# Kernel optimization log

Hardware: AMD Instinct MI355X
Metric: run time of the kernel (lower is better)

Reference implementation:

```python
import jax, jax.numpy as jnp
import numpy as np

B, L, E = 4, 2048, 1024
H, D = 16, 64  # heads, head_dim; H*D == E


def setup_inputs() -> dict:
    key = jax.random.key(0)
    ks = jax.random.split(key, 6)
    s = 0.02
    return {
        "x": jax.random.normal(ks[0], (B, L, E), dtype=jnp.float32),
        "Wq": jax.random.normal(ks[1], (E, H * D), dtype=jnp.float32) * s,
        "Wk": jax.random.normal(ks[2], (E, H * D), dtype=jnp.float32) * s,
        "Wv": jax.random.normal(ks[3], (E, H * D), dtype=jnp.float32) * s,
        "Wo": jax.random.normal(ks[4], (H * D, E), dtype=jnp.float32) * s,
        "bo": jax.random.normal(ks[5], (E,), dtype=jnp.float32) * s,
    }


def reference(x, Wq, Wk, Wv, Wo, bo):
    b, l, e = x.shape
    q = (x @ Wq).reshape(b, l, H, D)
    k = (x @ Wk).reshape(b, l, H, D)
    v = (x @ Wv).reshape(b, l, H, D)
    # NOTE: original scales by sqrt(embed_size), not sqrt(head_dim)
    energy = jnp.einsum('nqhd,nkhd->nhqk', q, k)
    attn = jax.nn.softmax(energy / jnp.sqrt(jnp.float32(e)), axis=3)
    out = jnp.einsum('nhql,nlhd->nqhd', attn, v).reshape(b, l, H * D)
    return out @ Wo + bo
```

## Files before the change

kernel.cpp:

```cpp
#include <hip/hip_runtime.h>

#define B_ 4
#define L_ 2048
#define E_ 1024
#define H_ 16
#define D_ 64
#define CSCALE 0.045084960222629414f

typedef short s16x8 __attribute__((ext_vector_type(8)));
typedef short s16x4 __attribute__((ext_vector_type(4)));
typedef float f32x4 __attribute__((ext_vector_type(4)));

__device__ __forceinline__ unsigned short f2bf(float f) {
  union { float f; unsigned int u; } v;
  v.f = f;
  unsigned int u = v.u;
  u += 0x7fffu + ((u >> 16) & 1u);
  return (unsigned short)(u >> 16);
}

__device__ __forceinline__ void async16(const void* g, void* l) {
  __builtin_amdgcn_global_load_lds(
      (__attribute__((address_space(1))) void*)(g),
      (__attribute__((address_space(3))) void*)(l), 16, 0, 0);
}

__global__ void k_prep(const float* __restrict__ x,
                       const float* __restrict__ Wq, const float* __restrict__ Wk,
                       const float* __restrict__ Wv, const float* __restrict__ Wo,
                       unsigned short* __restrict__ xb,
                       unsigned short* __restrict__ Wt, unsigned short* __restrict__ WoT) {
  __shared__ float t[32][33];
  int bid = blockIdx.x, tid = threadIdx.x;
  if (bid < 8192) {
    int i = bid * 256 + tid;
    float4 v = ((const float4*)x)[i];
    ushort4 o;
    o.x = f2bf(v.x); o.y = f2bf(v.y); o.z = f2bf(v.z); o.w = f2bf(v.w);
    ((ushort4*)xb)[i] = o;
    return;
  }
  int tt = bid - 8192;
  int wsel = tt >> 10, tile = tt & 1023;
  const float* in = (wsel == 0) ? Wq : (wsel == 1) ? Wk : (wsel == 2) ? Wv : Wo;
  unsigned short* out = (wsel == 0) ? Wt : (wsel == 1) ? Wt + (1u << 20)
                        : (wsel == 2) ? Wt + (2u << 20) : WoT;
  int bx = tile & 31, by = tile >> 5;
  int tx = tid & 31, ty = tid >> 5;
  int xcol = bx * 32 + tx;
  int y0 = by * 32;
#pragma unroll
  for (int i = 0; i < 4; ++i)
    t[ty + i * 8][tx] = in[(size_t)(y0 + ty + i * 8) * 1024 + xcol];
  __syncthreads();
  int xo = by * 32 + tx;
  int yo0 = bx * 32;
#pragma unroll
  for (int i = 0; i < 4; ++i)
    out[(size_t)(yo0 + ty + i * 8) * 1024 + xo] = f2bf(t[tx][ty + i * 8]);
}

__global__ __launch_bounds__(256) void k_gemm_qkvt(
    const unsigned short* __restrict__ xb, const unsigned short* __restrict__ Wt,
    unsigned short* __restrict__ Qb, unsigned short* __restrict__ Kb,
    unsigned short* __restrict__ Vt) {
  __shared__ __align__(16) unsigned short St[3][2][4096];
  const int bid0 = blockIdx.x;
  const int bid = (bid0 & 7) * 192 + (bid0 >> 3);
  const int tid = threadIdx.x;
  const int w = tid >> 6, lane = tid & 63;
  const int quad = lane >> 4, mrow = lane & 15;
  const bool isQK = bid < 1024;
  int m0, n0;
  const unsigned short *PA, *PB;
  if (isQK) {
    m0 = (bid & 63) * 128;
    n0 = (bid >> 6) * 128;
    PA = xb + (size_t)m0 * 1024;
    PB = Wt + (size_t)n0 * 1024;
  } else {
    int g = bid - 1024;
    m0 = (g & 7) * 128;
    n0 = (g >> 3) * 128;
    PA = Wt + (2u << 20) + (size_t)m0 * 1024;
    PB = xb + (size_t)n0 * 1024;
  }
  const int wr = (w >> 1) * 64, wc = (w & 1) * 64;

  auto issue = [&](int kt, int s) {
    int ktw = kt & 31;
#pragma unroll
    for (int r = 0; r < 2; ++r) {
      int c = r * 256 + tid;
      int row = c >> 2, cc = c & 3;
      async16(PA + (size_t)row * 1024 + ktw * 32 + cc * 8, &St[s][0][c * 8]);
      async16(PB + (size_t)row * 1024 + ktw * 32 + cc * 8, &St[s][1][c * 8]);
    }
  };

  const f32x4 fz = {0.f, 0.f, 0.f, 0.f};
  f32x4 acc[4][4];
#pragma unroll
  for (int a = 0; a < 4; ++a)
#pragma unroll
    for (int b = 0; b < 4; ++b) acc[a][b] = fz;

  issue(0, 0);
  issue(1, 1);

  for (int kt = 0; kt < 32; ++kt) {
    asm volatile("s_waitcnt vmcnt(4)" ::: "memory");
    __builtin_amdgcn_s_barrier();
    asm volatile("" ::: "memory");
    issue(kt + 2, (kt + 2) % 3);
    const unsigned short* As = &St[kt % 3][0][0];
    const unsigned short* Bs = &St[kt % 3][1][0];
    s16x8 a[4], b[4];
#pragma unroll
    for (int mt = 0; mt < 4; ++mt)
      a[mt] = *(const s16x8*)&As[(wr + mt * 16 + mrow) * 32 + quad * 8];
#pragma unroll
    for (int nt = 0; nt < 4; ++nt)
      b[nt] = *(const s16x8*)&Bs[(wc + nt * 16 + mrow) * 32 + quad * 8];
#pragma unroll
    for (int mt = 0; mt < 4; ++mt)
#pragma unroll
      for (int nt = 0; nt < 4; ++nt)
        acc[mt][nt] = __builtin_amdgcn_mfma_f32_16x16x32_bf16(a[mt], b[nt], acc[mt][nt], 0, 0, 0);
  }
  if (isQK) {
#pragma unroll
    for (int mt = 0; mt < 4; ++mt)
#pragma unroll
      for (int nt = 0; nt < 4; ++nt)
#pragma unroll
        for (int i = 0; i < 4; ++i) {
          int row = m0 + wr + mt * 16 + quad * 4 + i;
          int col = n0 + wc + nt * 16 + mrow;
          int bb = row >> 11, l = row & 2047;
          if (col < 1024) {
            int h = col >> 6, d = col & 63;
            Qb[(((size_t)(bb * 16 + h)) * 2048 + l) * 64 + d] = f2bf(acc[mt][nt][i]);
          } else {
            int c2 = col - 1024, h = c2 >> 6, d = c2 & 63;
            Kb[(((size_t)(bb * 16 + h)) * 2048 + l) * 64 + d] = f2bf(acc[mt][nt][i] * CSCALE);
          }
        }
  } else {
#pragma unroll
    for (int mt = 0; mt < 4; ++mt)
#pragma unroll
      for (int nt = 0; nt < 4; ++nt)
#pragma unroll
        for (int i = 0; i < 4; ++i) {
          int f = m0 + wr + mt * 16 + quad * 4 + i;
          int tk = n0 + wc + nt * 16 + mrow;
          int bb = tk >> 11, l = tk & 2047;
          Vt[((size_t)(bb * 1024 + f)) * 2048 + l] = f2bf(acc[mt][nt][i]);
        }
  }
}

struct AK { s16x8 k0, k1; };
struct ST { f32x4 s0, s1; };
struct PAT { s16x4 n0, n1; };

__device__ __forceinline__ AK load_ak(const unsigned short* Kt, int mt, int mrow, int quad) {
  int row = mt * 16 + mrow;
  AK r;
  r.k0 = *(const s16x8*)&Kt[row * 64 + (((0 + quad) ^ (row & 7)) << 3)];
  r.k1 = *(const s16x8*)&Kt[row * 64 + (((4 + quad) ^ (row & 7)) << 3)];
  return r;
}

__device__ __forceinline__ ST qkmm(const AK& a, const s16x8 (&qb)[2][2]) {
  const f32x4 fz = {0.f, 0.f, 0.f, 0.f};
  ST t; t.s0 = fz; t.s1 = fz;
  __builtin_amdgcn_s_setprio(1);
  t.s0 = __builtin_amdgcn_mfma_f32_16x16x32_bf16(a.k0, qb[0][0], t.s0, 0, 0, 0);
  t.s1 = __builtin_amdgcn_mfma_f32_16x16x32_bf16(a.k0, qb[1][0], t.s1, 0, 0, 0);
  t.s0 = __builtin_amdgcn_mfma_f32_16x16x32_bf16(a.k1, qb[0][1], t.s0, 0, 0, 0);
  t.s1 = __builtin_amdgcn_mfma_f32_16x16x32_bf16(a.k1, qb[1][1], t.s1, 0, 0, 0);
  __builtin_amdgcn_s_setprio(0);
  return t;
}

__device__ __forceinline__ s16x4 exp_pack(const f32x4 sv, float& lracc) {
  float p0 = __builtin_amdgcn_exp2f(sv[0]);
  float p1 = __builtin_amdgcn_exp2f(sv[1]);
  float p2 = __builtin_amdgcn_exp2f(sv[2]);
  float p3 = __builtin_amdgcn_exp2f(sv[3]);
  lracc += (p0 + p1) + (p2 + p3);
  unsigned int r01, r23;
  asm("v_cvt_pk_bf16_f32 %0, %1, %2" : "=v"(r01) : "v"(p0), "v"(p1));
  asm("v_cvt_pk_bf16_f32 %0, %1, %2" : "=v"(r23) : "v"(p2), "v"(p3));
  union { unsigned int u[2]; s16x4 v4; } uu;
  uu.u[0] = r01; uu.u[1] = r23;
  return uu.v4;
}

__device__ __forceinline__ PAT expp(const ST& t, float (&lr)[2]) {
  PAT r;
  r.n0 = exp_pack(t.s0, lr[0]);
  r.n1 = exp_pack(t.s1, lr[1]);
  return r;
}

__device__ __forceinline__ void pv(const unsigned short* Vs, int lt, const PAT& p,
                                   f32x4 (&o)[2][4], int mrow, int quad) {
  s16x4 vb[4];
  int lbase = lt * 16 + quad * 4;
  int cg = lbase >> 3, off = lbase & 7;
#pragma unroll
  for (int dt = 0; dt < 4; ++dt) {
    int row = dt * 16 + mrow;
    vb[dt] = *(const s16x4*)&Vs[row * 64 + ((cg ^ (row & 7)) << 3) + off];
  }
  __builtin_amdgcn_s_setprio(1);
#pragma unroll
  for (int dt = 0; dt < 4; ++dt) {
    o[0][dt] = __builtin_amdgcn_mfma_f32_16x16x16bf16_1k(p.n0, vb[dt], o[0][dt], 0, 0, 0);
    o[1][dt] = __builtin_amdgcn_mfma_f32_16x16x16bf16_1k(p.n1, vb[dt], o[1][dt], 0, 0, 0);
  }
  __builtin_amdgcn_s_setprio(0);
}

__global__ __launch_bounds__(512) void k_attn(
    const unsigned short* __restrict__ Qb, const unsigned short* __restrict__ Kb,
    const unsigned short* __restrict__ Vt, unsigned short* __restrict__ AO) {
  __shared__ __align__(16) unsigned short KVs[3][8192];
  const int tid = threadIdx.x, w = tid >> 6, lane = tid & 63;
  const int quad = lane >> 4, mrow = lane & 15;
  const int lin = blockIdx.x + 8 * blockIdx.y;
  const int swz = (lin & 7) * 64 + (lin >> 3);
  const int bh = swz >> 3;
  const int q0 = (swz & 7) * 256;
  const unsigned short* Qh = Qb + (size_t)bh * 2048 * 64;
  const unsigned short* Kh = Kb + (size_t)bh * 2048 * 64;
  const unsigned short* Vh = Vt + (size_t)bh * 64 * 2048;
  unsigned short* KVf = &KVs[0][0];

#pragma unroll
  for (int r = 0; r < 4; ++r) {
    int c = r * 512 + tid;
    int row = c >> 3, cl = c & 7;
    int gc = cl ^ (row & 7);
    async16(Qh + (size_t)(q0 + row) * 64 + gc * 8, &KVf[c * 8]);
  }
  asm volatile("s_waitcnt vmcnt(0)" ::: "memory");
  __builtin_amdgcn_s_barrier();
  asm volatile("" ::: "memory");
  s16x8 qb[2][2];
#pragma unroll
  for (int nt = 0; nt < 2; ++nt)
#pragma unroll
    for (int ks = 0; ks < 2; ++ks) {
      int row = w * 32 + nt * 16 + mrow;
      qb[nt][ks] = *(const s16x8*)&KVf[row * 64 + (((ks * 4 + quad) ^ (row & 7)) << 3)];
    }
  asm volatile("" ::: "memory");
  __builtin_amdgcn_s_barrier();
  asm volatile("" ::: "memory");

  {
    int row = tid >> 3, cl = tid & 7, gc = cl ^ (row & 7);
    async16(Kh + (size_t)row * 64 + gc * 8, &KVs[0][tid * 8]);
    async16(Vh + (size_t)row * 2048 + gc * 8, &KVs[0][4096 + tid * 8]);
    async16(Kh + (size_t)(64 + row) * 64 + gc * 8, &KVs[1][tid * 8]);
    async16(Vh + (size_t)row * 2048 + 64 + gc * 8, &KVs[1][4096 + tid * 8]);
  }

  const f32x4 fz = {0.f, 0.f, 0.f, 0.f};
  f32x4 o[2][4];
  float lr[2];
#pragma unroll
  for (int nt = 0; nt < 2; ++nt) {
    lr[nt] = 0.f;
#pragma unroll
    for (int dt = 0; dt < 4; ++dt) o[nt][dt] = fz;
  }

  for (int j = 0; j < 32; ++j) {
    asm volatile("s_waitcnt vmcnt(2)" ::: "memory");
    __builtin_amdgcn_s_barrier();
    asm volatile("" ::: "memory");
    {
      int jj = (j + 2) & 31;
      unsigned short* nb = &KVs[(j + 2) % 3][0];
      int row = tid >> 3, cl = tid & 7, gc = cl ^ (row & 7);
      async16(Kh + (size_t)(jj * 64 + row) * 64 + gc * 8, &nb[tid * 8]);
      async16(Vh + (size_t)row * 2048 + jj * 64 + gc * 8, &nb[4096 + tid * 8]);
    }
    const unsigned short* Kt = &KVs[j % 3][0];
    const unsigned short* Vs = &KVs[j % 3][4096];

    AK a0 = load_ak(Kt, 0, mrow, quad); ST t0 = qkmm(a0, qb);
    AK a1 = load_ak(Kt, 1, mrow, quad); ST t1 = qkmm(a1, qb);
    PAT p0 = expp(t0, lr);
    AK a2 = load_ak(Kt, 2, mrow, quad); ST t2 = qkmm(a2, qb);
    pv(Vs, 0, p0, o, mrow, quad);
    PAT p1 = expp(t1, lr);
    AK a3 = load_ak(Kt, 3, mrow, quad); ST t3 = qkmm(a3, qb);
    pv(Vs, 1, p1, o, mrow, quad);
    PAT p2 = expp(t2, lr);
    pv(Vs, 2, p2, o, mrow, quad);
    PAT p3 = expp(t3, lr);
    pv(Vs, 3, p3, o, mrow, quad);
  }

#pragma unroll
  for (int nt = 0; nt < 2; ++nt) {
    float v = lr[nt];
    v += __shfl_xor(v, 16);
    v += __shfl_xor(v, 32);
    lr[nt] = v;
  }

  int b_ = bh >> 4, h = bh & 15;
#pragma unroll
  for (int nt = 0; nt < 2; ++nt)
#pragma unroll
    for (int i = 0; i < 4; ++i) {
      float inv = 1.f / __shfl(lr[nt], quad * 4 + i, 64);
      int qrow = q0 + w * 32 + nt * 16 + quad * 4 + i;
#pragma unroll
      for (int dt = 0; dt < 4; ++dt) {
        int d = dt * 16 + mrow;
        AO[((size_t)(b_ * 2048 + qrow)) * 1024 + h * 64 + d] = f2bf(o[nt][dt][i] * inv);
      }
    }
}

__global__ __launch_bounds__(256) void k_gemm_out(
    const unsigned short* __restrict__ Ab, const unsigned short* __restrict__ WoT,
    const float* __restrict__ bo, float* __restrict__ out) {
  __shared__ __align__(16) unsigned short St[3][2][4096];
  const int tid = threadIdx.x;
  const int w = tid >> 6, lane = tid & 63;
  const int quad = lane >> 4, mrow = lane & 15;
  const int lin = blockIdx.x + 64 * blockIdx.y;
  const int swz = (lin & 7) * 64 + (lin >> 3);
  const int m0 = (swz & 63) * 128, n0 = (swz >> 6) * 128;
  const int wr = (w >> 1) * 64, wc = (w & 1) * 64;
  const unsigned short* PA = Ab + (size_t)m0 * 1024;
  const unsigned short* PB = WoT + (size_t)n0 * 1024;

  auto issue = [&](int kt, int s) {
    int ktw = kt & 31;
#pragma unroll
    for (int r = 0; r < 2; ++r) {
      int c = r * 256 + tid;
      int row = c >> 2, cc = c & 3;
      async16(PA + (size_t)row * 1024 + ktw * 32 + cc * 8, &St[s][0][c * 8]);
      async16(PB + (size_t)row * 1024 + ktw * 32 + cc * 8, &St[s][1][c * 8]);
    }
  };

  const f32x4 fz = {0.f, 0.f, 0.f, 0.f};
  f32x4 acc[4][4];
#pragma unroll
  for (int a = 0; a < 4; ++a)
#pragma unroll
    for (int b = 0; b < 4; ++b) acc[a][b] = fz;

  issue(0, 0);
  issue(1, 1);

  for (int kt = 0; kt < 32; ++kt) {
    asm volatile("s_waitcnt vmcnt(4)" ::: "memory");
    __builtin_amdgcn_s_barrier();
    asm volatile("" ::: "memory");
    issue(kt + 2, (kt + 2) % 3);
    const unsigned short* As = &St[kt % 3][0][0];
    const unsigned short* Bs = &St[kt % 3][1][0];
    s16x8 a[4], b[4];
#pragma unroll
    for (int mt = 0; mt < 4; ++mt)
      a[mt] = *(const s16x8*)&As[(wr + mt * 16 + mrow) * 32 + quad * 8];
#pragma unroll
    for (int nt = 0; nt < 4; ++nt)
      b[nt] = *(const s16x8*)&Bs[(wc + nt * 16 + mrow) * 32 + quad * 8];
#pragma unroll
    for (int mt = 0; mt < 4; ++mt)
#pragma unroll
      for (int nt = 0; nt < 4; ++nt)
        acc[mt][nt] = __builtin_amdgcn_mfma_f32_16x16x32_bf16(a[mt], b[nt], acc[mt][nt], 0, 0, 0);
  }
#pragma unroll
  for (int mt = 0; mt < 4; ++mt)
#pragma unroll
    for (int nt = 0; nt < 4; ++nt)
#pragma unroll
      for (int i = 0; i < 4; ++i) {
        int row = m0 + wr + mt * 16 + quad * 4 + i;
        int col = n0 + wc + nt * 16 + mrow;
        out[(size_t)row * 1024 + col] = acc[mt][nt][i] + bo[col];
      }
}

extern "C" void kernel_launch(void* const* d_in, const int* in_sizes, int n_in,
                              void* d_out, int out_size, void* d_ws, size_t ws_size,
                              hipStream_t stream) {
  const float* x  = (const float*)d_in[0];
  const float* Wq = (const float*)d_in[1];
  const float* Wk = (const float*)d_in[2];
  const float* Wv = (const float*)d_in[3];
  const float* Wo = (const float*)d_in[4];
  const float* bo = (const float*)d_in[5];
  float* out = (float*)d_out;

  char* ws = (char*)d_ws;
  const size_t MiB = 1u << 20;
  unsigned short* xb  = (unsigned short*)(ws);
  unsigned short* Wt  = (unsigned short*)(ws + 16 * MiB);
  unsigned short* WoT = (unsigned short*)(ws + 22 * MiB);
  unsigned short* Qb  = (unsigned short*)(ws + 24 * MiB);
  unsigned short* Kb  = (unsigned short*)(ws + 40 * MiB);
  unsigned short* Vt  = (unsigned short*)(ws + 56 * MiB);
  unsigned short* AO  = xb;

  k_prep<<<12288, 256, 0, stream>>>(x, Wq, Wk, Wv, Wo, xb, Wt, WoT);
  k_gemm_qkvt<<<1536, 256, 0, stream>>>(xb, Wt, Qb, Kb, Vt);
  k_attn<<<dim3(8, 64), 512, 0, stream>>>(Qb, Kb, Vt, AO);
  k_gemm_out<<<dim3(64, 8), 256, 0, stream>>>(AO, WoT, bo, out);
}
```

Before: 274.1 us.

## Retile projection GEMMs to 512 threads with XOR-swizzled LDS layout

The QKV projection GEMM now uses 256x128 tiles with 8 waves per block, which halves the grid. The output GEMM keeps 128x128 tiles but splits them across 8 waves of 32x64 each. Both kernels store LDS tiles with an XOR swizzle on the 16-byte chunk index to cut bank conflicts on the fragment reads. The wait counts are adjusted for the new number of loads per stage. Each wave now gets more reuse per loaded tile, but the QKV kernel launches fewer blocks and the output GEMM's waves each carry less MFMA work.

```diff
diff --git a/kernel.cpp b/kernel.cpp
--- a/kernel.cpp
+++ b/kernel.cpp
@@ -60,28 +60,28 @@
     out[(size_t)(yo0 + ty + i * 8) * 1024 + xo] = f2bf(t[tx][ty + i * 8]);
 }
 
-__global__ __launch_bounds__(256) void k_gemm_qkvt(
+__global__ __launch_bounds__(512) void k_gemm_qkvt(
     const unsigned short* __restrict__ xb, const unsigned short* __restrict__ Wt,
     unsigned short* __restrict__ Qb, unsigned short* __restrict__ Kb,
     unsigned short* __restrict__ Vt) {
-  __shared__ __align__(16) unsigned short St[3][2][4096];
+  __shared__ __align__(16) unsigned short St[3][12288];
   const int bid0 = blockIdx.x;
-  const int bid = (bid0 & 7) * 192 + (bid0 >> 3);
+  const int bid = (bid0 & 7) * 96 + (bid0 >> 3);
   const int tid = threadIdx.x;
   const int w = tid >> 6, lane = tid & 63;
   const int quad = lane >> 4, mrow = lane & 15;
-  const bool isQK = bid < 1024;
+  const bool isQK = bid < 512;
   int m0, n0;
   const unsigned short *PA, *PB;
   if (isQK) {
-    m0 = (bid & 63) * 128;
-    n0 = (bid >> 6) * 128;
+    m0 = (bid & 31) * 256;
+    n0 = (bid >> 5) * 128;
     PA = xb + (size_t)m0 * 1024;
     PB = Wt + (size_t)n0 * 1024;
   } else {
-    int g = bid - 1024;
-    m0 = (g & 7) * 128;
-    n0 = (g >> 3) * 128;
+    int g = bid - 512;
+    m0 = (g & 3) * 256;
+    n0 = (g >> 2) * 128;
     PA = Wt + (2u << 20) + (size_t)m0 * 1024;
     PB = xb + (size_t)n0 * 1024;
   }
@@ -91,10 +91,14 @@
     int ktw = kt & 31;
 #pragma unroll
     for (int r = 0; r < 2; ++r) {
-      int c = r * 256 + tid;
-      int row = c >> 2, cc = c & 3;
-      async16(PA + (size_t)row * 1024 + ktw * 32 + cc * 8, &St[s][0][c * 8]);
-      async16(PB + (size_t)row * 1024 + ktw * 32 + cc * 8, &St[s][1][c * 8]);
+      int c = r * 512 + tid;
+      int row = c >> 2, cl = c & 3, gc = cl ^ (row & 3);
+      async16(PA + (size_t)row * 1024 + ktw * 32 + gc * 8, &St[s][c * 8]);
+    }
+    {
+      int c = tid;
+      int row = c >> 2, cl = c & 3, gc = cl ^ (row & 3);
+      async16(PB + (size_t)row * 1024 + ktw * 32 + gc * 8, &St[s][8192 + c * 8]);
     }
   };
 
@@ -109,19 +113,23 @@
   issue(1, 1);
 
   for (int kt = 0; kt < 32; ++kt) {
-    asm volatile("s_waitcnt vmcnt(4)" ::: "memory");
+    asm volatile("s_waitcnt vmcnt(3)" ::: "memory");
     __builtin_amdgcn_s_barrier();
     asm volatile("" ::: "memory");
     issue(kt + 2, (kt + 2) % 3);
-    const unsigned short* As = &St[kt % 3][0][0];
-    const unsigned short* Bs = &St[kt % 3][1][0];
+    const unsigned short* As = &St[kt % 3][0];
+    const unsigned short* Bs = &St[kt % 3][8192];
     s16x8 a[4], b[4];
 #pragma unroll
-    for (int mt = 0; mt < 4; ++mt)
-      a[mt] = *(const s16x8*)&As[(wr + mt * 16 + mrow) * 32 + quad * 8];
-#pragma unroll
-    for (int nt = 0; nt < 4; ++nt)
-      b[nt] = *(const s16x8*)&Bs[(wc + nt * 16 + mrow) * 32 + quad * 8];
+    for (int mt = 0; mt < 4; ++mt) {
+      int row = wr + mt * 16 + mrow;
+      a[mt] = *(const s16x8*)&As[row * 32 + ((quad ^ (row & 3)) << 3)];
+    }
+#pragma unroll
+    for (int nt = 0; nt < 4; ++nt) {
+      int row = wc + nt * 16 + mrow;
+      b[nt] = *(const s16x8*)&Bs[row * 32 + ((quad ^ (row & 3)) << 3)];
+    }
 #pragma unroll
     for (int mt = 0; mt < 4; ++mt)
 #pragma unroll
@@ -331,35 +339,38 @@
     }
 }
 
-__global__ __launch_bounds__(256) void k_gemm_out(
+__global__ __launch_bounds__(512) void k_gemm_out(
     const unsigned short* __restrict__ Ab, const unsigned short* __restrict__ WoT,
     const float* __restrict__ bo, float* __restrict__ out) {
-  __shared__ __align__(16) unsigned short St[3][2][4096];
+  __shared__ __align__(16) unsigned short St[3][8192];
   const int tid = threadIdx.x;
   const int w = tid >> 6, lane = tid & 63;
   const int quad = lane >> 4, mrow = lane & 15;
   const int lin = blockIdx.x + 64 * blockIdx.y;
   const int swz = (lin & 7) * 64 + (lin >> 3);
   const int m0 = (swz & 63) * 128, n0 = (swz >> 6) * 128;
-  const int wr = (w >> 1) * 64, wc = (w & 1) * 64;
+  const int wr = (w >> 1) * 32, wc = (w & 1) * 64;
   const unsigned short* PA = Ab + (size_t)m0 * 1024;
   const unsigned short* PB = WoT + (size_t)n0 * 1024;
 
   auto issue = [&](int kt, int s) {
     int ktw = kt & 31;
-#pragma unroll
-    for (int r = 0; r < 2; ++r) {
-      int c = r * 256 + tid;
-      int row = c >> 2, cc = c & 3;
-      async16(PA + (size_t)row * 1024 + ktw * 32 + cc * 8, &St[s][0][c * 8]);
-      async16(PB + (size_t)row * 1024 + ktw * 32 + cc * 8, &St[s][1][c * 8]);
+    {
+      int c = tid;
+      int row = c >> 2, cl = c & 3, gc = cl ^ (row & 3);
+      async16(PA + (size_t)row * 1024 + ktw * 32 + gc * 8, &St[s][c * 8]);
+    }
+    {
+      int c = tid;
+      int row = c >> 2, cl = c & 3, gc = cl ^ (row & 3);
+      async16(PB + (size_t)row * 1024 + ktw * 32 + gc * 8, &St[s][4096 + c * 8]);
     }
   };
 
   const f32x4 fz = {0.f, 0.f, 0.f, 0.f};
-  f32x4 acc[4][4];
-#pragma unroll
-  for (int a = 0; a < 4; ++a)
+  f32x4 acc[2][4];
+#pragma unroll
+  for (int a = 0; a < 2; ++a)
 #pragma unroll
     for (int b = 0; b < 4; ++b) acc[a][b] = fz;
 
@@ -367,27 +378,31 @@
   issue(1, 1);
 
   for (int kt = 0; kt < 32; ++kt) {
-    asm volatile("s_waitcnt vmcnt(4)" ::: "memory");
+    asm volatile("s_waitcnt vmcnt(2)" ::: "memory");
     __builtin_amdgcn_s_barrier();
     asm volatile("" ::: "memory");
     issue(kt + 2, (kt + 2) % 3);
-    const unsigned short* As = &St[kt % 3][0][0];
-    const unsigned short* Bs = &St[kt % 3][1][0];
-    s16x8 a[4], b[4];
-#pragma unroll
-    for (int mt = 0; mt < 4; ++mt)
-      a[mt] = *(const s16x8*)&As[(wr + mt * 16 + mrow) * 32 + quad * 8];
-#pragma unroll
-    for (int nt = 0; nt < 4; ++nt)
-      b[nt] = *(const s16x8*)&Bs[(wc + nt * 16 + mrow) * 32 + quad * 8];
-#pragma unroll
-    for (int mt = 0; mt < 4; ++mt)
+    const unsigned short* As = &St[kt % 3][0];
+    const unsigned short* Bs = &St[kt % 3][4096];
+    s16x8 a[2], b[4];
+#pragma unroll
+    for (int mt = 0; mt < 2; ++mt) {
+      int row = wr + mt * 16 + mrow;
+      a[mt] = *(const s16x8*)&As[row * 32 + ((quad ^ (row & 3)) << 3)];
+    }
+#pragma unroll
+    for (int nt = 0; nt < 4; ++nt) {
+      int row = wc + nt * 16 + mrow;
+      b[nt] = *(const s16x8*)&Bs[row * 32 + ((quad ^ (row & 3)) << 3)];
+    }
+#pragma unroll
+    for (int mt = 0; mt < 2; ++mt)
 #pragma unroll
       for (int nt = 0; nt < 4; ++nt)
         acc[mt][nt] = __builtin_amdgcn_mfma_f32_16x16x32_bf16(a[mt], b[nt], acc[mt][nt], 0, 0, 0);
   }
 #pragma unroll
-  for (int mt = 0; mt < 4; ++mt)
+  for (int mt = 0; mt < 2; ++mt)
 #pragma unroll
     for (int nt = 0; nt < 4; ++nt)
 #pragma unroll
@@ -420,7 +435,7 @@
   unsigned short* AO  = xb;
 
   k_prep<<<12288, 256, 0, stream>>>(x, Wq, Wk, Wv, Wo, xb, Wt, WoT);
-  k_gemm_qkvt<<<1536, 256, 0, stream>>>(xb, Wt, Qb, Kb, Vt);
+  k_gemm_qkvt<<<768, 512, 0, stream>>>(xb, Wt, Qb, Kb, Vt);
   k_attn<<<dim3(8, 64), 512, 0, stream>>>(Qb, Kb, Vt, AO);
-  k_gemm_out<<<dim3(64, 8), 256, 0, stream>>>(AO, WoT, bo, out);
-}
+  k_gemm_out<<<dim3(64, 8), 512, 0, stream>>>(AO, WoT, bo, out);
+}
```

Result: no change. 269.0 us (-1.9%).
